# Performance work log

Hardware: AMD Instinct MI355X
Metric: run time of the kernel (lower is better)

Reference implementation:

```python
import jax, jax.numpy as jnp
import numpy as np
import math

B, R, C = 4, 512, 512
E, H, D, M, F = 256, 16, 16, 16, 512  # embed, heads, qkv_dim, ms_hidden, ff_hidden
EPS = 1e-5


def setup_inputs() -> dict:
    key = jax.random.key(0)
    ks = jax.random.split(key, 20)
    s = lambda fan_in: 1.0 / math.sqrt(fan_in)
    u = lambda k, shape, lim: jax.random.uniform(k, shape, jnp.float32, -lim, lim)
    mix1_init = (1 / 2) ** 0.5
    mix2_init = (1 / 16) ** 0.5
    return {
        "row_emb": jax.random.normal(ks[0], (B, R, E), jnp.float32),
        "col_emb": jax.random.normal(ks[1], (B, C, E), jnp.float32),
        "cost_mat": jax.random.uniform(ks[2], (B, R, C), jnp.float32),
        "Wq": u(ks[3], (E, H * D), s(E)),
        "Wk": u(ks[4], (E, H * D), s(E)),
        "Wv": u(ks[5], (E, H * D), s(E)),
        "mix1_w": u(ks[6], (H, 2, M), mix1_init),
        "mix1_b": u(ks[7], (H, M), mix1_init),
        "mix2_w": u(ks[8], (H, M, 1), mix2_init),
        "mix2_b": u(ks[9], (H, 1), mix2_init),
        "Wc": u(ks[10], (H * D, E), s(H * D)),
        "bc": u(ks[11], (E,), s(H * D)),
        "W1": u(ks[12], (E, F), s(E)),
        "b1": u(ks[13], (F,), s(E)),
        "W2": u(ks[14], (F, E), s(F)),
        "b2": u(ks[15], (E,), s(F)),
        "g1": jnp.ones((E,), jnp.float32),
        "be1": jnp.zeros((E,), jnp.float32),
        "g2": jnp.ones((E,), jnp.float32),
        "be2": jnp.zeros((E,), jnp.float32),
    }


def _instance_norm(x, gamma, beta):
    # InstanceNorm1d on x permuted to (B, E, L): normalize over seq dim per (b, channel)
    mean = jnp.mean(x, axis=1, keepdims=True)          # [B,1,E]
    var = jnp.mean((x - mean) ** 2, axis=1, keepdims=True)
    return (x - mean) * jax.lax.rsqrt(var + EPS) * gamma + beta


def reference(row_emb, col_emb, cost_mat, Wq, Wk, Wv, mix1_w, mix1_b, mix2_w,
              mix2_b, Wc, bc, W1, b1, W2, b2, g1, be1, g2, be2):
    # QKV projections, split heads: [B,L,H*D] -> [B,H,L,D]
    q = (row_emb @ Wq).reshape(B, R, H, D).transpose(0, 2, 1, 3)
    k = (col_emb @ Wk).reshape(B, C, H, D).transpose(0, 2, 1, 3)
    v = (col_emb @ Wv).reshape(B, C, H, D).transpose(0, 2, 1, 3)

    dot = jnp.einsum('bhrd,bhcd->bhrc', q, k) / math.sqrt(D)
    cost = jnp.broadcast_to(cost_mat[:, None, :, :], (B, H, R, C))
    two = jnp.stack((dot, cost), axis=-1)               # [B,H,R,C,2]

    # per-head 2 -> M -> 1 mixing MLP over scores
    ms1 = jnp.einsum('bhrcs,hsm->bhrcm', two, mix1_w) + mix1_b[None, :, None, None, :]
    ms1 = jax.nn.relu(ms1)
    mixed = jnp.einsum('bhrcm,hm->bhrc', ms1, mix2_w[:, :, 0]) + mix2_b[:, 0][None, :, None, None]

    weights = jax.nn.softmax(mixed, axis=-1)            # [B,H,R,C]
    out = jnp.einsum('bhrc,bhcd->bhrd', weights, v)
    out_concat = out.transpose(0, 2, 1, 3).reshape(B, R, H * D)

    mh = out_concat @ Wc + bc                           # multi_head_combine

    # TransformerFFN with instance norm
    x = _instance_norm(row_emb + mh, g1, be1)
    ffn = jax.nn.relu(x @ W1 + b1) @ W2 + b2
    return _instance_norm(x + ffn, g2, be2)
```

## Files before the change

kernel.cpp:

```cpp
#include <hip/hip_runtime.h>
#include <hip/hip_bf16.h>

typedef __hip_bfloat16 bf16;
typedef __hip_bfloat162 bf162;
typedef _Float16 f16;
typedef __attribute__((ext_vector_type(2))) _Float16 h2;
typedef __attribute__((ext_vector_type(8))) short short8;
typedef __attribute__((ext_vector_type(4))) float f32x4;

#define B_ 4
#define R_ 512
#define C_ 512
#define E_ 256
#define H_ 16
#define D_ 16

__device__ __forceinline__ float b2f(bf16 x) { return __bfloat162float(x); }
__device__ __forceinline__ void stout(bf16* p, float v) { *p = __float2bfloat16(v); }
__device__ __forceinline__ void stout(f16* p, float v) { *p = (f16)v; }

__global__ __launch_bounds__(256) void transpose_cvt_kernel(
    const float* __restrict__ Wq, const float* __restrict__ Wk, const float* __restrict__ Wv,
    const float* __restrict__ Wc, const float* __restrict__ W1, const float* __restrict__ W2,
    bf16* __restrict__ WqT, bf16* __restrict__ WkT, bf16* __restrict__ WvT,
    bf16* __restrict__ WcT, bf16* __restrict__ W1T, bf16* __restrict__ W2T,
    float* __restrict__ statsZ)
{
    __shared__ bf16 tile[32][33];
    const int wsel = blockIdx.y;
    const int tx = blockIdx.x;
    if (wsel == 0 && tx >= 64) {
        const int idx = (tx - 64) * 256 + threadIdx.x;
        if (idx < 4096) statsZ[idx] = 0.f;
        return;
    }
    const float* src; bf16* dst; int K, N; float scl = 1.0f;
    switch (wsel) {
        case 0: src = Wq; dst = WqT; K = 256; N = 256; scl = 0.25f; break;
        case 1: src = Wk; dst = WkT; K = 256; N = 256; break;
        case 2: src = Wv; dst = WvT; K = 256; N = 256; break;
        case 3: src = Wc; dst = WcT; K = 256; N = 256; break;
        case 4: src = W1; dst = W1T; K = 256; N = 512; break;
        default: src = W2; dst = W2T; K = 512; N = 256; break;
    }
    const int ntiles = (K >> 5) * (N >> 5);
    if (tx >= ntiles) return;
    const int ncnt = N >> 5;
    const int tk = tx / ncnt, tn = tx % ncnt;
    const int c = threadIdx.x & 31, r = threadIdx.x >> 5;
#pragma unroll
    for (int i = 0; i < 4; i++)
        tile[r + i * 8][c] = __float2bfloat16(scl * src[(size_t)(tk * 32 + r + i * 8) * N + tn * 32 + c]);
    __syncthreads();
#pragma unroll
    for (int i = 0; i < 4; i++)
        dst[(size_t)(tn * 32 + r + i * 8) * K + tk * 32 + c] = tile[c][r + i * 8];
}

template <int AMODE, typename OT, int BM, int BN, bool BIAS, int RES, bool RELU, bool STATS>
__device__ __forceinline__ void mfma_gemm_body(
    const void* __restrict__ Ap, const bf16* __restrict__ BT,
    const float* __restrict__ bias, const void* __restrict__ Res,
    const float* __restrict__ normS, const float* __restrict__ normG, const float* __restrict__ normB,
    float* __restrict__ statsOut, OT* __restrict__ Cout,
    int M, int N, int K, int bx, int by)
{
    constexpr int MT = BM / 32, NT = BN / 32;
    constexpr int AEL = BM * 64 / 256, BEL = BN * 64 / 256;
    __shared__ __align__(16) bf16 As[BM * 80];
    __shared__ __align__(16) bf16 Bs[BN * 80];
    const int tid = threadIdx.x;
    const int wid = tid >> 6, lane = tid & 63;
    const int wm = wid >> 1, wn = wid & 1;
    const int fr = lane & 15, quad = lane >> 4;
    const int m0 = by * BM, n0 = bx * BN;
    const int arow = (AEL == 16) ? (tid >> 2) : (tid >> 3);
    const int akg  = (AEL == 16) ? ((tid & 3) << 4) : ((tid & 7) << 3);
    const int brow = (BEL == 16) ? (tid >> 2) : (tid >> 3);
    const int bkg  = (BEL == 16) ? ((tid & 3) << 4) : ((tid & 7) << 3);

    f32x4 acc[MT][NT];
#pragma unroll
    for (int mt = 0; mt < MT; mt++)
#pragma unroll
        for (int nt = 0; nt < NT; nt++) acc[mt][nt] = (f32x4){0.f, 0.f, 0.f, 0.f};

    for (int k0 = 0; k0 < K; k0 += 64) {
        if constexpr (AMODE == 0) {
            const short8* gp = (const short8*)((const bf16*)Ap + (size_t)(m0 + arow) * K + k0 + akg);
#pragma unroll
            for (int t8 = 0; t8 < AEL / 8; t8++) *(short8*)(&As[arow * 80 + akg + 8 * t8]) = gp[t8];
        } else if constexpr (AMODE == 1) {
            const float4* gp = (const float4*)((const float*)Ap + (size_t)(m0 + arow) * K + k0 + akg);
#pragma unroll
            for (int j = 0; j < AEL / 4; j++) {
                const float4 f = gp[j];
                *(bf162*)(&As[arow * 80 + akg + j * 4])     = __float22bfloat162_rn(make_float2(f.x, f.y));
                *(bf162*)(&As[arow * 80 + akg + j * 4 + 2]) = __float22bfloat162_rn(make_float2(f.z, f.w));
            }
        } else {
            const int bb = (m0 + arow) >> 9;
            const bf16* ap = (const bf16*)Ap + (size_t)(m0 + arow) * K + k0 + akg;
            bf16 tmp[AEL];
#pragma unroll
            for (int t8 = 0; t8 < AEL / 8; t8++) *(short8*)(tmp + 8 * t8) = ((const short8*)ap)[t8];
#pragma unroll
            for (int j = 0; j < AEL; j++) {
                const int e = k0 + akg + j;
                const float s = normS[bb * 256 + e], sq = normS[1024 + bb * 256 + e];
                const float mn = s * (1.f / 512.f);
                float var = sq * (1.f / 512.f) - mn * mn; var = fmaxf(var, 0.f);
                As[arow * 80 + akg + j] = __float2bfloat16(
                    (b2f(tmp[j]) - mn) * rsqrtf(var + 1e-5f) * normG[e] + normB[e]);
            }
        }
        {
            const short8* gp = (const short8*)(BT + (size_t)(n0 + brow) * K + k0 + bkg);
#pragma unroll
            for (int t8 = 0; t8 < BEL / 8; t8++) *(short8*)(&Bs[brow * 80 + bkg + 8 * t8]) = gp[t8];
        }
        __syncthreads();

        short8 af[MT][2], bfr[NT][2];
#pragma unroll
        for (int mt = 0; mt < MT; mt++) {
            const int ar = wm * (BM / 2) + mt * 16 + fr;
#pragma unroll
            for (int kh = 0; kh < 2; kh++)
                af[mt][kh] = *(const short8*)(&As[ar * 80 + quad * 8 + kh * 32]);
        }
#pragma unroll
        for (int nt = 0; nt < NT; nt++) {
            const int br = wn * (BN / 2) + nt * 16 + fr;
#pragma unroll
            for (int kh = 0; kh < 2; kh++)
                bfr[nt][kh] = *(const short8*)(&Bs[br * 80 + quad * 8 + kh * 32]);
        }
#pragma unroll
        for (int kh = 0; kh < 2; kh++)
#pragma unroll
            for (int mt = 0; mt < MT; mt++)
#pragma unroll
                for (int nt = 0; nt < NT; nt++)
                    acc[mt][nt] = __builtin_amdgcn_mfma_f32_16x16x32_bf16(
                        af[mt][kh], bfr[nt][kh], acc[mt][nt], 0, 0, 0);
        __syncthreads();
    }

    float vsum[NT], vss[NT];
#pragma unroll
    for (int nt = 0; nt < NT; nt++) { vsum[nt] = 0.f; vss[nt] = 0.f; }
#pragma unroll
    for (int mt = 0; mt < MT; mt++) {
#pragma unroll
        for (int nt = 0; nt < NT; nt++) {
#pragma unroll
            for (int i = 0; i < 4; i++) {
                const int row = m0 + wm * (BM / 2) + mt * 16 + quad * 4 + i;
                const int col = n0 + wn * (BN / 2) + nt * 16 + fr;
                float v = acc[mt][nt][i];
                if (BIAS) v += bias[col];
                if constexpr (RES == 1) v += ((const float*)Res)[(size_t)row * N + col];
                if constexpr (RES == 3) {
                    const int bb = row >> 9;
                    const float yv = b2f(((const bf16*)Res)[(size_t)row * N + col]);
                    const float s = normS[bb * 256 + col], sq = normS[1024 + bb * 256 + col];
                    const float mn = s * (1.f / 512.f);
                    float var = sq * (1.f / 512.f) - mn * mn; var = fmaxf(var, 0.f);
                    v += (yv - mn) * rsqrtf(var + 1e-5f) * normG[col] + normB[col];
                }
                if (RELU) v = fmaxf(v, 0.f);
                stout(&Cout[(size_t)row * N + col], v);
                if (STATS) { vsum[nt] += v; vss[nt] += v * v; }
            }
        }
    }
    if constexpr (STATS) {
        float* sred = (float*)As;
#pragma unroll
        for (int nt = 0; nt < NT; nt++) {
            float a = vsum[nt]; a += __shfl_xor(a, 16, 64); a += __shfl_xor(a, 32, 64);
            float c = vss[nt];  c += __shfl_xor(c, 16, 64); c += __shfl_xor(c, 32, 64);
            if (quad == 0) {
                const int cl = wn * (BN / 2) + nt * 16 + fr;
                sred[wm * (2 * BN) + cl * 2 + 0] = a;
                sred[wm * (2 * BN) + cl * 2 + 1] = c;
            }
        }
        __syncthreads();
        if (tid < 2 * BN) {
            const int cl = tid >> 1, w = tid & 1;
            const float tot = sred[cl * 2 + w] + sred[2 * BN + cl * 2 + w];
            atomicAdd(&statsOut[w * 1024 + (m0 >> 9) * 256 + n0 + cl], tot);
        }
    }
}

template <int AMODE, typename OT, int BM, int BN, bool BIAS, int RES, bool RELU, bool STATS>
__global__ __launch_bounds__(256) void mfma_gemm_kernel(
    const void* __restrict__ Ap, const bf16* __restrict__ BT,
    const float* __restrict__ bias, const void* __restrict__ Res,
    const float* __restrict__ normS, const float* __restrict__ normG, const float* __restrict__ normB,
    float* __restrict__ statsOut, OT* __restrict__ Cout, int M, int N, int K)
{
    mfma_gemm_body<AMODE, OT, BM, BN, BIAS, RES, RELU, STATS>(
        Ap, BT, bias, Res, normS, normG, normB, statsOut, Cout,
        M, N, K, blockIdx.x, blockIdx.y);
}

__global__ __launch_bounds__(256) void qkv_kernel(
    const float* __restrict__ rowE, const float* __restrict__ colE,
    const bf16* __restrict__ WqT, const bf16* __restrict__ WkT, const bf16* __restrict__ WvT,
    f16* __restrict__ qo, f16* __restrict__ ko, bf16* __restrict__ vo)
{
    const int z = blockIdx.z;
    if (z == 2) {
        mfma_gemm_body<1, bf16, 32, 64, false, 0, false, false>(
            colE, WvT, nullptr, nullptr, nullptr, nullptr, nullptr, nullptr, vo,
            2048, 256, 256, blockIdx.x, blockIdx.y);
    } else {
        mfma_gemm_body<1, f16, 32, 64, false, 0, false, false>(
            (z == 0) ? rowE : colE, (z == 0) ? WqT : WkT,
            nullptr, nullptr, nullptr, nullptr, nullptr, nullptr, (z == 0) ? qo : ko,
            2048, 256, 256, blockIdx.x, blockIdx.y);
    }
}

__global__ __launch_bounds__(256) void attn_kernel(
    const f16* __restrict__ q, const f16* __restrict__ k, const bf16* __restrict__ v,
    const float* __restrict__ cost, const float* __restrict__ m1w, const float* __restrict__ m1b,
    const float* __restrict__ m2w, const float* __restrict__ m2b,
    bf16* __restrict__ po, float* __restrict__ plf)
{
    __shared__ __align__(16) f16 kbuf[128 * 16];
    __shared__ __align__(16) short vbuf[128 * 16];

    const int rt = blockIdx.x >> 2, cs = blockIdx.x & 3;
    const int h = blockIdx.y, b = blockIdx.z;
    const int tid = threadIdx.x, wid = tid >> 6, lane = tid & 63;
    const int quad = lane >> 4, fr = lane & 15;

    {
        const size_t base = ((size_t)b * C_) * 256 + h * 16 + (size_t)cs * 128 * 256;
        const int lc = tid >> 1, dp = (tid & 1) * 8;
        const size_t g = base + (size_t)lc * 256 + dp;
        *(short8*)(&kbuf[lc * 16 + dp]) = *(const short8*)(k + g);
        *(short8*)(&vbuf[lc * 16 + dp]) = *(const short8*)(v + g);
    }

    h2 w1a2[8], w1b2[8], b1h[8], w2p[8];
#pragma unroll
    for (int i = 0; i < 8; i++) {
        h2 t;
        t.x = (f16)m1w[h * 32 + 2 * i];      t.y = (f16)m1w[h * 32 + 2 * i + 1];      w1a2[i] = t;
        t.x = (f16)m1w[h * 32 + 16 + 2 * i]; t.y = (f16)m1w[h * 32 + 17 + 2 * i];     w1b2[i] = t;
        t.x = (f16)m1b[h * 16 + 2 * i];      t.y = (f16)m1b[h * 16 + 2 * i + 1];      b1h[i] = t;
        t.x = (f16)m2w[h * 16 + 2 * i];      t.y = (f16)m2w[h * 16 + 2 * i + 1];      w2p[i] = t;
    }
    const float b2v = m2b[h];
    const h2 zero2 = (h2)(f16)0;

    const int row_m = rt * 64 + wid * 16 + fr;
    short8 qraw[2];
    {
        const short8* qp = (const short8*)(q + (size_t)(b * R_ + row_m) * 256 + h * 16);
        qraw[0] = qp[0]; qraw[1] = qp[1];
    }
    const h2* qh = (const h2*)qraw;

    __syncthreads();

    const float* crow = cost + (size_t)(b * R_ + row_m) * C_ + cs * 128;
    h2 sh[16];
#pragma unroll
    for (int blk = 0; blk < 4; blk++) {
        const float4 c0 = *(const float4*)(crow + blk * 32 + quad * 8);
        const float4 c1 = *(const float4*)(crow + blk * 32 + quad * 8 + 4);
        const float carr[8] = {c0.x, c0.y, c0.z, c0.w, c1.x, c1.y, c1.z, c1.w};
#pragma unroll
        for (int j = 0; j < 8; j++) {
            const int col = blk * 32 + quad * 8 + j;
            const h2* kr = (const h2*)(&kbuf[col * 16]);
            h2 dacc = qh[0] * kr[0];
#pragma unroll
            for (int i = 1; i < 8; i++) dacc = qh[i] * kr[i] + dacc;
            const float dot = (float)dacc.x + (float)dacc.y;
            const float cst = carr[j];
            const f16 doth = (f16)dot, csth = (f16)cst;
            h2 dot2; dot2.x = doth; dot2.y = doth;
            h2 cst2; cst2.x = csth; cst2.y = csth;
            h2 acc2 = (h2)(f16)0;
#pragma unroll
            for (int i = 0; i < 8; i++) {
                h2 t = dot2 * w1a2[i] + b1h[i];
                t = cst2 * w1b2[i] + t;
                t = __builtin_elementwise_max(t, zero2);
                acc2 = t * w2p[i] + acc2;
            }
            const float s = b2v + (float)acc2.x + (float)acc2.y;
            const f16 sf = (f16)s;
            if (j & 1) sh[blk * 4 + (j >> 1)].y = sf;
            else       sh[blk * 4 + (j >> 1)].x = sf;
        }
    }

    h2 mx2 = sh[0];
#pragma unroll
    for (int i = 1; i < 16; i++) mx2 = __builtin_elementwise_max(mx2, sh[i]);
    float m_l = fmaxf((float)mx2.x, (float)mx2.y);
    m_l = fmaxf(m_l, __shfl_xor(m_l, 16, 64));
    m_l = fmaxf(m_l, __shfl_xor(m_l, 32, 64));

    f32x4 oacc = (f32x4){0.f, 0.f, 0.f, 0.f};
    float lsum = 0.f;
#pragma unroll
    for (int blk = 0; blk < 4; blk++) {
        short8 pa, bv;
#pragma unroll
        for (int jj = 0; jj < 4; jj++) {
            const h2 t = sh[blk * 4 + jj];
            const float e0 = __expf((float)t.x - m_l);
            const float e1 = __expf((float)t.y - m_l);
            lsum += e0 + e1;
            const bf162 pr = __float22bfloat162_rn(make_float2(e0, e1));
            pa[2 * jj]     = __builtin_bit_cast(short, pr.x);
            pa[2 * jj + 1] = __builtin_bit_cast(short, pr.y);
        }
#pragma unroll
        for (int j = 0; j < 8; j++) bv[j] = vbuf[(blk * 32 + quad * 8 + j) * 16 + fr];
        oacc = __builtin_amdgcn_mfma_f32_16x16x32_bf16(pa, bv, oacc, 0, 0, 0);
    }
    lsum += __shfl_xor(lsum, 16, 64);
    lsum += __shfl_xor(lsum, 32, 64);

    const int idxbase = cs * 32768 + ((b * H_ + h) << 9) + rt * 64 + wid * 16;
    if (quad == 0) plf[idxbase + fr] = lsum * __expf(m_l);
#pragma unroll
    for (int i = 0; i < 4; i++) {
        const float li = __shfl(lsum, quad * 4 + i, 64);
        po[(size_t)(idxbase + quad * 4 + i) * 16 + fr] = __float2bfloat16(oacc[i] / li);
    }
}

__global__ __launch_bounds__(256) void attn_merge_kernel(
    const bf16* __restrict__ po, const float* __restrict__ plf, bf16* __restrict__ sa)
{
    const int idx = blockIdx.x * 256 + threadIdx.x;
    const float l0 = plf[idx], l1 = plf[32768 + idx];
    const float l2 = plf[65536 + idx], l3 = plf[98304 + idx];
    const float inv = 1.f / (l0 + l1 + l2 + l3);
    float oo[16] = {};
#pragma unroll
    for (int c = 0; c < 4; c++) {
        const float wgt = ((c == 0) ? l0 : (c == 1) ? l1 : (c == 2) ? l2 : l3) * inv;
        const bf162* pp = (const bf162*)(po + (size_t)(c * 32768 + idx) * 16);
#pragma unroll
        for (int j = 0; j < 8; j++) {
            const float2 f = __bfloat1622float2(pp[j]);
            oo[2 * j]     = fmaf(wgt, f.x, oo[2 * j]);
            oo[2 * j + 1] = fmaf(wgt, f.y, oo[2 * j + 1]);
        }
    }
    const int b = idx >> 13, h = (idx >> 9) & 15, r = idx & 511;
    bf162* dst = (bf162*)(sa + (size_t)(b * R_ + r) * 256 + h * 16);
#pragma unroll
    for (int j = 0; j < 8; j++)
        dst[j] = __float22bfloat162_rn(make_float2(oo[2 * j], oo[2 * j + 1]));
}

__global__ __launch_bounds__(256) void apply_in2_kernel(
    const bf16* __restrict__ xin, const float* __restrict__ stats,
    const float* __restrict__ g, const float* __restrict__ be, float* __restrict__ outp)
{
    const int base = (blockIdx.x * 256 + threadIdx.x) * 4;
    const int b = base >> 17;
    const bf162* xp = (const bf162*)(xin + base);
    const float2 x0 = __bfloat1622float2(xp[0]), x1 = __bfloat1622float2(xp[1]);
    const float xv[4] = {x0.x, x0.y, x1.x, x1.y};
    float4 rr;
    float* rp = (float*)&rr;
#pragma unroll
    for (int j = 0; j < 4; j++) {
        const int e = (base & 255) + j;
        const float s = stats[b * 256 + e], sq = stats[1024 + b * 256 + e];
        const float mn = s * (1.f / 512.f);
        float var = sq * (1.f / 512.f) - mn * mn; var = fmaxf(var, 0.f);
        rp[j] = (xv[j] - mn) * rsqrtf(var + 1e-5f) * g[e] + be[e];
    }
    *(float4*)(outp + base) = rr;
}

extern "C" void kernel_launch(void* const* d_in, const int* in_sizes, int n_in,
                              void* d_out, int out_size, void* d_ws, size_t ws_size,
                              hipStream_t stream)
{
    (void)in_sizes; (void)n_in; (void)out_size; (void)ws_size;
    const float* row_emb = (const float*)d_in[0];
    const float* col_emb = (const float*)d_in[1];
    const float* cost    = (const float*)d_in[2];
    const float* Wq  = (const float*)d_in[3];
    const float* Wk  = (const float*)d_in[4];
    const float* Wv  = (const float*)d_in[5];
    const float* m1w = (const float*)d_in[6];
    const float* m1b = (const float*)d_in[7];
    const float* m2w = (const float*)d_in[8];
    const float* m2b = (const float*)d_in[9];
    const float* Wc  = (const float*)d_in[10];
    const float* bc  = (const float*)d_in[11];
    const float* W1  = (const float*)d_in[12];
    const float* b1  = (const float*)d_in[13];
    const float* W2  = (const float*)d_in[14];
    const float* b2  = (const float*)d_in[15];
    const float* g1  = (const float*)d_in[16];
    const float* be1 = (const float*)d_in[17];
    const float* g2  = (const float*)d_in[18];
    const float* be2 = (const float*)d_in[19];
    float* out = (float*)d_out;

    char* w = (char*)d_ws;
    const size_t MB = 1u << 20;
    f16*  sq  = (f16*)(w + 0 * MB);
    f16*  sk  = (f16*)(w + 1 * MB);
    bf16* sv  = (bf16*)(w + 2 * MB);
    bf16* sa  = (bf16*)(w + 0 * MB);
    bf16* sy  = (bf16*)(w + 1 * MB);
    bf16* st  = (bf16*)(w + 2 * MB);
    bf16* po  = (bf16*)(w + 3 * MB);
    bf16* shm = (bf16*)(w + 3 * MB);
    float* plf = (float*)(w + 7 * MB);
    bf16* WqT = (bf16*)(w + 8 * MB);
    bf16* WkT = WqT + 65536;
    bf16* WvT = WkT + 65536;
    bf16* WcT = WvT + 65536;
    bf16* W1T = WcT + 65536;
    bf16* W2T = W1T + 131072;
    float* stats1 = (float*)(w + 9 * MB);
    float* stats2 = stats1 + 2048;

    const dim3 blk(256);

    transpose_cvt_kernel<<<dim3(128, 6), blk, 0, stream>>>(
        Wq, Wk, Wv, Wc, W1, W2, WqT, WkT, WvT, WcT, W1T, W2T, stats1);

    qkv_kernel<<<dim3(4, 64, 3), blk, 0, stream>>>(row_emb, col_emb, WqT, WkT, WvT, sq, sk, sv);

    attn_kernel<<<dim3(32, 16, 4), blk, 0, stream>>>(
        sq, sk, sv, cost, m1w, m1b, m2w, m2b, po, plf);

    attn_merge_kernel<<<dim3(128), blk, 0, stream>>>(po, plf, sa);

    mfma_gemm_kernel<0, bf16, 32, 32, true, 1, false, true><<<dim3(8, 64), blk, 0, stream>>>(
        sa, WcT, bc, row_emb, nullptr, nullptr, nullptr, stats1, sy, 2048, 256, 256);

    mfma_gemm_kernel<2, bf16, 32, 64, true, 0, true, false><<<dim3(8, 64), blk, 0, stream>>>(
        sy, W1T, b1, nullptr, stats1, g1, be1, nullptr, shm, 2048, 512, 256);

    mfma_gemm_kernel<0, bf16, 32, 32, true, 3, false, true><<<dim3(8, 64), blk, 0, stream>>>(
        shm, W2T, b2, sy, stats1, g1, be1, stats2, st, 2048, 256, 512);

    apply_in2_kernel<<<dim3(512), blk, 0, stream>>>(st, stats2, g2, be2, out);
}
```

Before: 161.0 us.

## Fuse split-column attention with merge using online softmax and MFMA QK scores

Each attention block now processes all 512 columns, with an online-softmax rescale across four 128-column chunks, so the separate merge kernel and its partial-output round trip through global memory go away. The per-lane scalar QK dot products become f16 16x16x16 MFMA instructions reading a swizzled K tile. V is stored as f16 and transposed into LDS for the PV MFMA. Cost rows are prefetched into a double buffer. The grid shrinks by a factor of four (512 blocks) while LDS use per block grows, which may reduce occupancy and parallelism.

Measured after the change: 153.2 us. 4.9% less time.

```diff
diff --git a/kernel.cpp b/kernel.cpp
--- a/kernel.cpp
+++ b/kernel.cpp
@@ -5,7 +5,9 @@
 typedef __hip_bfloat162 bf162;
 typedef _Float16 f16;
 typedef __attribute__((ext_vector_type(2))) _Float16 h2;
+typedef __attribute__((ext_vector_type(4))) _Float16 f16x4;
 typedef __attribute__((ext_vector_type(8))) short short8;
+typedef __attribute__((ext_vector_type(4))) short short4v;
 typedef __attribute__((ext_vector_type(4))) float f32x4;
 
 #define B_ 4
@@ -211,41 +213,45 @@
 __global__ __launch_bounds__(256) void qkv_kernel(
     const float* __restrict__ rowE, const float* __restrict__ colE,
     const bf16* __restrict__ WqT, const bf16* __restrict__ WkT, const bf16* __restrict__ WvT,
-    f16* __restrict__ qo, f16* __restrict__ ko, bf16* __restrict__ vo)
+    f16* __restrict__ qo, f16* __restrict__ ko, f16* __restrict__ vo)
 {
     const int z = blockIdx.z;
-    if (z == 2) {
-        mfma_gemm_body<1, bf16, 32, 64, false, 0, false, false>(
-            colE, WvT, nullptr, nullptr, nullptr, nullptr, nullptr, nullptr, vo,
-            2048, 256, 256, blockIdx.x, blockIdx.y);
-    } else {
-        mfma_gemm_body<1, f16, 32, 64, false, 0, false, false>(
-            (z == 0) ? rowE : colE, (z == 0) ? WqT : WkT,
-            nullptr, nullptr, nullptr, nullptr, nullptr, nullptr, (z == 0) ? qo : ko,
-            2048, 256, 256, blockIdx.x, blockIdx.y);
-    }
+    const float* A = (z == 0) ? rowE : colE;
+    const bf16* BT = (z == 0) ? WqT : (z == 1) ? WkT : WvT;
+    f16* out = (z == 0) ? qo : (z == 1) ? ko : vo;
+    mfma_gemm_body<1, f16, 32, 64, false, 0, false, false>(
+        A, BT, nullptr, nullptr, nullptr, nullptr, nullptr, nullptr, out,
+        2048, 256, 256, blockIdx.x, blockIdx.y);
 }
 
 __global__ __launch_bounds__(256) void attn_kernel(
-    const f16* __restrict__ q, const f16* __restrict__ k, const bf16* __restrict__ v,
+    const f16* __restrict__ q, const f16* __restrict__ k, const f16* __restrict__ v,
     const float* __restrict__ cost, const float* __restrict__ m1w, const float* __restrict__ m1b,
     const float* __restrict__ m2w, const float* __restrict__ m2b,
-    bf16* __restrict__ po, float* __restrict__ plf)
-{
-    __shared__ __align__(16) f16 kbuf[128 * 16];
-    __shared__ __align__(16) short vbuf[128 * 16];
-
-    const int rt = blockIdx.x >> 2, cs = blockIdx.x & 3;
-    const int h = blockIdx.y, b = blockIdx.z;
+    bf16* __restrict__ sa)
+{
+    __shared__ __align__(16) short kbuf[512 * 16];
+    __shared__ __align__(16) _Float16 vbufT[16 * 520];
+
+    const int rt = blockIdx.x, h = blockIdx.y, b = blockIdx.z;
     const int tid = threadIdx.x, wid = tid >> 6, lane = tid & 63;
     const int quad = lane >> 4, fr = lane & 15;
+    const int row_m = rt * 64 + wid * 16 + fr;
+
+    const f16x4 qf = *(const f16x4*)(q + (size_t)(b * R_ + row_m) * 256 + h * 16 + (quad << 2));
 
     {
-        const size_t base = ((size_t)b * C_) * 256 + h * 16 + (size_t)cs * 128 * 256;
-        const int lc = tid >> 1, dp = (tid & 1) * 8;
-        const size_t g = base + (size_t)lc * 256 + dp;
-        *(short8*)(&kbuf[lc * 16 + dp]) = *(const short8*)(k + g);
-        *(short8*)(&vbuf[lc * 16 + dp]) = *(const short8*)(v + g);
+        const int lc0 = tid >> 1, dp = (tid & 1) * 8;
+        const size_t gbase = (size_t)(b * C_) * 256 + h * 16 + dp;
+#pragma unroll
+        for (int it = 0; it < 4; it++) {
+            const int lc = it * 128 + lc0;
+            const size_t g = gbase + (size_t)lc * 256;
+            *(short8*)(&kbuf[lc * 16 + (dp ^ ((lc & 1) << 3))]) = *(const short8*)(k + g);
+            const short8 vv = *(const short8*)(v + g);
+#pragma unroll
+            for (int u = 0; u < 8; u++) vbufT[(dp + u) * 520 + lc] = ((const _Float16*)&vv)[u];
+        }
     }
 
     h2 w1a2[8], w1b2[8], b1h[8], w2p[8];
@@ -260,112 +266,83 @@
     const float b2v = m2b[h];
     const h2 zero2 = (h2)(f16)0;
 
-    const int row_m = rt * 64 + wid * 16 + fr;
-    short8 qraw[2];
-    {
-        const short8* qp = (const short8*)(q + (size_t)(b * R_ + row_m) * 256 + h * 16);
-        qraw[0] = qp[0]; qraw[1] = qp[1];
-    }
-    const h2* qh = (const h2*)qraw;
+    const float* crow = cost + (size_t)(b * R_ + row_m) * C_;
+    float4 cf[2][8];
+#pragma unroll
+    for (int t = 0; t < 8; t++) cf[0][t] = *(const float4*)(crow + t * 16 + (quad << 2));
 
     __syncthreads();
 
-    const float* crow = cost + (size_t)(b * R_ + row_m) * C_ + cs * 128;
-    h2 sh[16];
-#pragma unroll
-    for (int blk = 0; blk < 4; blk++) {
-        const float4 c0 = *(const float4*)(crow + blk * 32 + quad * 8);
-        const float4 c1 = *(const float4*)(crow + blk * 32 + quad * 8 + 4);
-        const float carr[8] = {c0.x, c0.y, c0.z, c0.w, c1.x, c1.y, c1.z, c1.w};
-#pragma unroll
-        for (int j = 0; j < 8; j++) {
-            const int col = blk * 32 + quad * 8 + j;
-            const h2* kr = (const h2*)(&kbuf[col * 16]);
-            h2 dacc = qh[0] * kr[0];
-#pragma unroll
-            for (int i = 1; i < 8; i++) dacc = qh[i] * kr[i] + dacc;
-            const float dot = (float)dacc.x + (float)dacc.y;
-            const float cst = carr[j];
-            const f16 doth = (f16)dot, csth = (f16)cst;
-            h2 dot2; dot2.x = doth; dot2.y = doth;
-            h2 cst2; cst2.x = csth; cst2.y = csth;
-            h2 acc2 = (h2)(f16)0;
-#pragma unroll
-            for (int i = 0; i < 8; i++) {
-                h2 t = dot2 * w1a2[i] + b1h[i];
-                t = cst2 * w1b2[i] + t;
-                t = __builtin_elementwise_max(t, zero2);
-                acc2 = t * w2p[i] + acc2;
-            }
-            const float s = b2v + (float)acc2.x + (float)acc2.y;
-            const f16 sf = (f16)s;
-            if (j & 1) sh[blk * 4 + (j >> 1)].y = sf;
-            else       sh[blk * 4 + (j >> 1)].x = sf;
-        }
-    }
-
-    h2 mx2 = sh[0];
-#pragma unroll
-    for (int i = 1; i < 16; i++) mx2 = __builtin_elementwise_max(mx2, sh[i]);
-    float m_l = fmaxf((float)mx2.x, (float)mx2.y);
-    m_l = fmaxf(m_l, __shfl_xor(m_l, 16, 64));
-    m_l = fmaxf(m_l, __shfl_xor(m_l, 32, 64));
-
-    f32x4 oacc = (f32x4){0.f, 0.f, 0.f, 0.f};
-    float lsum = 0.f;
-#pragma unroll
-    for (int blk = 0; blk < 4; blk++) {
-        short8 pa, bv;
-#pragma unroll
-        for (int jj = 0; jj < 4; jj++) {
-            const h2 t = sh[blk * 4 + jj];
-            const float e0 = __expf((float)t.x - m_l);
-            const float e1 = __expf((float)t.y - m_l);
-            lsum += e0 + e1;
-            const bf162 pr = __float22bfloat162_rn(make_float2(e0, e1));
-            pa[2 * jj]     = __builtin_bit_cast(short, pr.x);
-            pa[2 * jj + 1] = __builtin_bit_cast(short, pr.y);
-        }
-#pragma unroll
-        for (int j = 0; j < 8; j++) bv[j] = vbuf[(blk * 32 + quad * 8 + j) * 16 + fr];
-        oacc = __builtin_amdgcn_mfma_f32_16x16x32_bf16(pa, bv, oacc, 0, 0, 0);
-    }
+    f32x4 oaccT = (f32x4){0.f, 0.f, 0.f, 0.f};
+    float lsum = 0.f, m_run = -3.0e30f;
+
+#pragma unroll
+    for (int cs = 0; cs < 4; cs++) {
+        if (cs < 3) {
+#pragma unroll
+            for (int t = 0; t < 8; t++)
+                cf[(cs + 1) & 1][t] = *(const float4*)(crow + (cs + 1) * 128 + t * 16 + (quad << 2));
+        }
+        f32x4 sc[8];
+#pragma unroll
+        for (int t = 0; t < 8; t++) {
+            const int c = cs * 128 + t * 16 + fr;
+            const f16x4 kf = *(const f16x4*)(&kbuf[c * 16 + ((quad << 2) ^ ((fr & 1) << 3))]);
+            sc[t] = __builtin_amdgcn_mfma_f32_16x16x16f16(kf, qf, (f32x4){0.f, 0.f, 0.f, 0.f}, 0, 0, 0);
+        }
+#pragma unroll
+        for (int t = 0; t < 8; t++) {
+            const float4 cq = cf[cs & 1][t];
+            const float carr[4] = {cq.x, cq.y, cq.z, cq.w};
+#pragma unroll
+            for (int i = 0; i < 4; i++) {
+                const f16 doth = (f16)sc[t][i], csth = (f16)carr[i];
+                h2 dot2; dot2.x = doth; dot2.y = doth;
+                h2 cst2; cst2.x = csth; cst2.y = csth;
+                h2 acc2 = zero2;
+#pragma unroll
+                for (int mm = 0; mm < 8; mm++) {
+                    h2 tt = dot2 * w1a2[mm] + b1h[mm];
+                    tt = cst2 * w1b2[mm] + tt;
+                    tt = __builtin_elementwise_max(tt, zero2);
+                    acc2 = tt * w2p[mm] + acc2;
+                }
+                sc[t][i] = b2v + (float)acc2.x + (float)acc2.y;
+            }
+        }
+        float mx = fmaxf(fmaxf(sc[0][0], sc[0][1]), fmaxf(sc[0][2], sc[0][3]));
+#pragma unroll
+        for (int t = 1; t < 8; t++)
+            mx = fmaxf(mx, fmaxf(fmaxf(sc[t][0], sc[t][1]), fmaxf(sc[t][2], sc[t][3])));
+        mx = fmaxf(mx, __shfl_xor(mx, 16, 64));
+        mx = fmaxf(mx, __shfl_xor(mx, 32, 64));
+        const float mnew = fmaxf(m_run, mx);
+        const float fac = __expf(m_run - mnew);
+        m_run = mnew;
+        lsum *= fac;
+        oaccT[0] *= fac; oaccT[1] *= fac; oaccT[2] *= fac; oaccT[3] *= fac;
+
+#pragma unroll
+        for (int p = 0; p < 8; p++) {
+            f16x4 pf;
+#pragma unroll
+            for (int j = 0; j < 4; j++) {
+                const float e = __expf(sc[p][j] - m_run);
+                lsum += e;
+                pf[j] = (f16)e;
+            }
+            const f16x4 vf = *(const f16x4*)(&vbufT[fr * 520 + cs * 128 + p * 16 + (quad << 2)]);
+            oaccT = __builtin_amdgcn_mfma_f32_16x16x16f16(vf, pf, oaccT, 0, 0, 0);
+        }
+    }
+
     lsum += __shfl_xor(lsum, 16, 64);
     lsum += __shfl_xor(lsum, 32, 64);
-
-    const int idxbase = cs * 32768 + ((b * H_ + h) << 9) + rt * 64 + wid * 16;
-    if (quad == 0) plf[idxbase + fr] = lsum * __expf(m_l);
-#pragma unroll
-    for (int i = 0; i < 4; i++) {
-        const float li = __shfl(lsum, quad * 4 + i, 64);
-        po[(size_t)(idxbase + quad * 4 + i) * 16 + fr] = __float2bfloat16(oacc[i] / li);
-    }
-}
-
-__global__ __launch_bounds__(256) void attn_merge_kernel(
-    const bf16* __restrict__ po, const float* __restrict__ plf, bf16* __restrict__ sa)
-{
-    const int idx = blockIdx.x * 256 + threadIdx.x;
-    const float l0 = plf[idx], l1 = plf[32768 + idx];
-    const float l2 = plf[65536 + idx], l3 = plf[98304 + idx];
-    const float inv = 1.f / (l0 + l1 + l2 + l3);
-    float oo[16] = {};
-#pragma unroll
-    for (int c = 0; c < 4; c++) {
-        const float wgt = ((c == 0) ? l0 : (c == 1) ? l1 : (c == 2) ? l2 : l3) * inv;
-        const bf162* pp = (const bf162*)(po + (size_t)(c * 32768 + idx) * 16);
-#pragma unroll
-        for (int j = 0; j < 8; j++) {
-            const float2 f = __bfloat1622float2(pp[j]);
-            oo[2 * j]     = fmaf(wgt, f.x, oo[2 * j]);
-            oo[2 * j + 1] = fmaf(wgt, f.y, oo[2 * j + 1]);
-        }
-    }
-    const int b = idx >> 13, h = (idx >> 9) & 15, r = idx & 511;
-    bf162* dst = (bf162*)(sa + (size_t)(b * R_ + r) * 256 + h * 16);
-#pragma unroll
-    for (int j = 0; j < 8; j++)
-        dst[j] = __float22bfloat162_rn(make_float2(oo[2 * j], oo[2 * j + 1]));
+    const float inv = 1.f / lsum;
+    short4v o;
+#pragma unroll
+    for (int i = 0; i < 4; i++) o[i] = __builtin_bit_cast(short, __float2bfloat16(oaccT[i] * inv));
+    *(short4v*)((short*)sa + (size_t)(b * R_ + row_m) * 256 + h * 16 + (quad << 2)) = o;
 }
 
 __global__ __launch_bounds__(256) void apply_in2_kernel(
@@ -421,13 +398,11 @@
     const size_t MB = 1u << 20;
     f16*  sq  = (f16*)(w + 0 * MB);
     f16*  sk  = (f16*)(w + 1 * MB);
-    bf16* sv  = (bf16*)(w + 2 * MB);
-    bf16* sa  = (bf16*)(w + 0 * MB);
-    bf16* sy  = (bf16*)(w + 1 * MB);
-    bf16* st  = (bf16*)(w + 2 * MB);
-    bf16* po  = (bf16*)(w + 3 * MB);
-    bf16* shm = (bf16*)(w + 3 * MB);
-    float* plf = (float*)(w + 7 * MB);
+    f16*  sv  = (f16*)(w + 2 * MB);
+    bf16* sa  = (bf16*)(w + 3 * MB);
+    bf16* sy  = (bf16*)(w + 4 * MB);
+    bf16* st  = (bf16*)(w + 5 * MB);
+    bf16* shm = (bf16*)(w + 6 * MB);
     bf16* WqT = (bf16*)(w + 8 * MB);
     bf16* WkT = WqT + 65536;
     bf16* WvT = WkT + 65536;
@@ -444,10 +419,8 @@
 
     qkv_kernel<<<dim3(4, 64, 3), blk, 0, stream>>>(row_emb, col_emb, WqT, WkT, WvT, sq, sk, sv);
 
-    attn_kernel<<<dim3(32, 16, 4), blk, 0, stream>>>(
-        sq, sk, sv, cost, m1w, m1b, m2w, m2b, po, plf);
-
-    attn_merge_kernel<<<dim3(128), blk, 0, stream>>>(po, plf, sa);
+    attn_kernel<<<dim3(8, 16, 4), blk, 0, stream>>>(
+        sq, sk, sv, cost, m1w, m1b, m2w, m2b, sa);
 
     mfma_gemm_kernel<0, bf16, 32, 32, true, 1, false, true><<<dim3(8, 64), blk, 0, stream>>>(
         sa, WcT, bc, row_emb, nullptr, nullptr, nullptr, stats1, sy, 2048, 256, 256);
```
